# Kernel tuning notes

Hardware: AMD Instinct MI355X
Metric: run time of the kernel (lower is better)

The kernel has to match this reference:

```python
import jax, jax.numpy as jnp
import numpy as np

D_MODEL = 96
N_HEAD = 3
HEAD_DIM = D_MODEL // N_HEAD  # 32
D_FF = 2048
WIDTH = 65
HALF_W = (WIDTH - 1) // 2  # 32
EPS = 1e-5


def layer_norm(x, g, b):
    mu = jnp.mean(x, axis=-1, keepdims=True)
    var = jnp.mean(jnp.square(x - mu), axis=-1, keepdims=True)
    return (x - mu) * jax.lax.rsqrt(var + EPS) * g + b


def setup_inputs() -> dict:
    key = jax.random.key(0)
    ks = jax.random.split(key, 8)
    B, T = 8, 2048
    s = 0.05
    return {
        "x": jax.random.normal(ks[0], (B, D_MODEL, T), dtype=jnp.float32),
        "w_qkv": jax.random.normal(ks[1], (3 * D_MODEL, D_MODEL), dtype=jnp.float32) * s,
        "b_qkv": jnp.zeros((3 * D_MODEL,), dtype=jnp.float32),
        "w_out": jax.random.normal(ks[2], (D_MODEL, D_MODEL), dtype=jnp.float32) * s,
        "b_out": jnp.zeros((D_MODEL,), dtype=jnp.float32),
        "ln1_g": jnp.ones((D_MODEL,), dtype=jnp.float32),
        "ln1_b": jnp.zeros((D_MODEL,), dtype=jnp.float32),
        "w_ff1": jax.random.normal(ks[3], (D_FF, D_MODEL), dtype=jnp.float32) * s,
        "b_ff1": jnp.zeros((D_FF,), dtype=jnp.float32),
        "w_ff2": jax.random.normal(ks[4], (D_MODEL, D_FF), dtype=jnp.float32) * s,
        "b_ff2": jnp.zeros((D_MODEL,), dtype=jnp.float32),
        "ln2_g": jnp.ones((D_MODEL,), dtype=jnp.float32),
        "ln2_b": jnp.zeros((D_MODEL,), dtype=jnp.float32),
        "lnf_g": jnp.ones((D_MODEL,), dtype=jnp.float32),
        "lnf_b": jnp.zeros((D_MODEL,), dtype=jnp.float32),
    }


def reference(x, w_qkv, b_qkv, w_out, b_out, ln1_g, ln1_b, w_ff1, b_ff1,
              w_ff2, b_ff2, ln2_g, ln2_b, lnf_g, lnf_b):
    # x: (B, C, T) -> (B, T, C)
    h = jnp.transpose(x, (0, 2, 1))
    B, T, C = h.shape

    # --- multi-head self-attention with banded mask ---
    qkv = h @ w_qkv.T + b_qkv                      # (B, T, 3C)
    q, k, v = jnp.split(qkv, 3, axis=-1)
    q = q.reshape(B, T, N_HEAD, HEAD_DIM)
    k = k.reshape(B, T, N_HEAD, HEAD_DIM)
    v = v.reshape(B, T, N_HEAD, HEAD_DIM)

    scale = 1.0 / jnp.sqrt(jnp.float32(HEAD_DIM))
    scores = jnp.einsum("bthd,bshd->bhts", q, k) * scale  # (B, H, T, T)

    idx = jnp.arange(T)
    band = jnp.abs(idx[:, None] - idx[None, :]) <= HALF_W  # |i-j| <= half width
    scores = jnp.where(band[None, None], scores, jnp.float32(-jnp.inf))

    attn = jax.nn.softmax(scores, axis=-1)
    ctx = jnp.einsum("bhts,bshd->bthd", attn, v).reshape(B, T, C)
    attn_out = ctx @ w_out.T + b_out

    # --- post-norm encoder layer (dropout inactive / eval mode) ---
    h = layer_norm(h + attn_out, ln1_g, ln1_b)
    ff = jax.nn.relu(h @ w_ff1.T + b_ff1) @ w_ff2.T + b_ff2
    h = layer_norm(h + ff, ln2_g, ln2_b)

    # extra layernorm applied when width is not None
    h = layer_norm(h, lnf_g, lnf_b)

    # (B, T, C) -> (B, C, T)
    return jnp.transpose(h, (0, 2, 1))
```

## Files before the change

### kernel.cpp

```cpp
#include <hip/hip_runtime.h>
#include <hip/hip_bf16.h>

#define B 8
#define T 2048
#define C 96
#define NH 3
#define HD 32
#define FFD 2048
#define HALF_W 32
#define BT (B*T)

typedef __hip_bfloat16 bf16;
typedef __attribute__((ext_vector_type(8))) short short8;
typedef __attribute__((ext_vector_type(4))) short short4v;
typedef __attribute__((ext_vector_type(16))) float floatx16;

__device__ __forceinline__ short f2bs(float v){
    __hip_bfloat16 h = __float2bfloat16(v);
    return *reinterpret_cast<short*>(&h);
}
__device__ __forceinline__ int imin(int a, int b){ return a < b ? a : b; }
__device__ __forceinline__ int imax(int a, int b){ return a > b ? a : b; }
__device__ __forceinline__ short8 ld_b64x2(const short* p){
    short4v a = *(const short4v*)p;
    short4v b = *(const short4v*)(p + 4);
    short8 v;
    v[0]=a[0]; v[1]=a[1]; v[2]=a[2]; v[3]=a[3];
    v[4]=b[0]; v[5]=b[1]; v[6]=b[2]; v[7]=b[3];
    return v;
}

__global__ void cvtw_kernel(const float* __restrict__ wq, const float* __restrict__ wo,
                            const float* __restrict__ w1, const float* __restrict__ w2,
                            bf16* __restrict__ dst){
    int i = blockIdx.x*256 + threadIdx.x;
    if(i < 27648){
        int e = i&7, lane = (i>>3)&63, r = i>>9;
        int ks = r%6, ot = r/6;
        int o = ot*32 + (lane&31);
        int k = ks*16 + (lane>>5)*8 + e;
        dst[i] = __float2bfloat16(wq[o*96 + k]);
    } else if(i < 36864){
        int j = i - 27648;
        int e = j&7, lane = (j>>3)&63, r = j>>9;
        int ks = r%6, ct = r/6;
        int c = ct*32 + (lane&31);
        int k = ks*16 + (lane>>5)*8 + e;
        dst[i] = __float2bfloat16(wo[c*96 + k]);
    } else if(i < 233472){
        int j = i - 36864;
        int e = j&7, lane = (j>>3)&63, r = j>>9;
        int ks = r%6; r /= 6;
        int w = r%4, jt = r/4;
        int row = jt*128 + w*32 + (lane&31);
        int k = ks*16 + (lane>>5)*8 + e;
        dst[i] = __float2bfloat16(w1[row*96 + k]);
    } else if(i < 430080){
        int j = i - 233472;
        int e = j&7, lane = (j>>3)&63, r = j>>9;
        int ct = r%3; r /= 3;
        int g = r%2; r /= 2;
        int w = r%4, jt = r/4;
        int c = ct*32 + (lane&31);
        int k = jt*128 + w*32 + g*16 + (lane>>5)*8 + e;
        dst[i] = __float2bfloat16(w2[c*FFD + k]);
    }
}

__global__ __launch_bounds__(256) void qkv_kernel(
    const float* __restrict__ x, const bf16* __restrict__ wqs,
    const float* __restrict__ bias, bf16* __restrict__ qkvs){
    __shared__ float xs[96*36];
    int b  = blockIdx.x >> 6;
    int t0 = (blockIdx.x & 63) * 32;
    for(int e = threadIdx.x; e < 96*8; e += 256){
        int c = e >> 3, t4 = e & 7;
        *(float4*)(xs + c*36 + t4*4) =
            *(const float4*)(x + (size_t)b*C*T + (size_t)c*T + t0 + t4*4);
    }
    __syncthreads();
    int r0 = b*T + t0;
    const int w = threadIdx.x >> 6, lane = threadIdx.x & 63;
    const int lm = lane & 31, hq = lane >> 5;
    short8 bfr[6];
    #pragma unroll
    for(int ks = 0; ks < 6; ++ks){
        short8 v;
        #pragma unroll
        for(int i = 0; i < 8; ++i)
            v[i] = f2bs(xs[(ks*16 + hq*8 + i)*36 + lm]);
        bfr[ks] = v;
    }
    int nacc = (w == 0) ? 3 : 2;
    int ots[3] = {w, w+4, 8};
    floatx16 acc[3];
    #pragma unroll
    for(int i = 0; i < 3; ++i)
        #pragma unroll
        for(int r = 0; r < 16; ++r) acc[i][r] = 0.f;
    #pragma unroll
    for(int i = 0; i < 3; ++i){
        if(i < nacc){
            #pragma unroll
            for(int ks = 0; ks < 6; ++ks){
                short8 af = *(const short8*)((const short*)wqs
                              + (size_t)(ots[i]*6 + ks)*512 + lane*8);
                acc[i] = __builtin_amdgcn_mfma_f32_32x32x16_bf16(af, bfr[ks], acc[i], 0,0,0);
            }
        }
    }
    #pragma unroll
    for(int i = 0; i < 3; ++i){
        if(i < nacc){
            int type = ots[i]/3, hh = ots[i]%3;
            size_t rowbase = (((size_t)type*B*NH) + (size_t)b*NH + hh)*T + t0 + lm;
            #pragma unroll
            for(int q = 0; q < 4; ++q){
                float4 bv = *(const float4*)(bias + ots[i]*32 + 8*q + 4*hq);
                short4v pk;
                pk[0] = f2bs(acc[i][4*q+0] + bv.x);
                pk[1] = f2bs(acc[i][4*q+1] + bv.y);
                pk[2] = f2bs(acc[i][4*q+2] + bv.z);
                pk[3] = f2bs(acc[i][4*q+3] + bv.w);
                *(short4v*)((short*)qkvs + rowbase*32 + 8*q + 4*hq) = pk;
            }
        }
    }
}

__global__ __launch_bounds__(128) void attn_kernel(const bf16* __restrict__ qkvs,
                                                   bf16* __restrict__ ctxh){
    __shared__ __align__(16) short VtS[32*132];
    __shared__ __align__(16) short PtS[2][32*100];
    __shared__ float LsS[2][32];
    int blk = blockIdx.x;
    int ntile = T/64;
    int b   = blk / (NH*ntile);
    int rem = blk % (NH*ntile);
    int h   = rem / ntile;
    int t0  = (rem % ntile) * 64;
    const short* qb = (const short*)qkvs + ((size_t)0*B*NH + (size_t)b*NH + h)*T*32;
    const short* kb = (const short*)qkvs + ((size_t)1*B*NH + (size_t)b*NH + h)*T*32;
    const short* vb = (const short*)qkvs + ((size_t)2*B*NH + (size_t)b*NH + h)*T*32;
    const int tid = threadIdx.x;
    const int w = tid >> 6, lane = tid & 63;
    const int lm = lane & 31, hq = lane >> 5;

    for(int e = tid; e < 256; e += 128){
        int kp = e >> 2, d8 = e & 3;
        int sa = imin(imax(t0 - 32 + 2*kp, 0), T-1);
        int sb = imin(imax(t0 - 32 + 2*kp + 1, 0), T-1);
        short8 va = *(const short8*)(vb + (size_t)sa*32 + d8*8);
        short8 v2 = *(const short8*)(vb + (size_t)sb*32 + d8*8);
        #pragma unroll
        for(int j = 0; j < 8; ++j){
            int val = (int)(unsigned short)va[j] | ((int)(unsigned short)v2[j] << 16);
            *(int*)(VtS + (d8*8 + j)*132 + 2*kp) = val;
        }
    }
    short8 qf0, qf1;
    {
        const short* qrow = qb + (size_t)(t0 + 32*w + lm)*32;
        qf0 = *(const short8*)(qrow + hq*8);
        qf1 = *(const short8*)(qrow + 16 + hq*8);
    }
    floatx16 S[3];
    #pragma unroll
    for(int sub = 0; sub < 3; ++sub){
        int srow = imin(imax(t0 + 32*w - 32 + sub*32 + lm, 0), T-1);
        const short* krow = kb + (size_t)srow*32;
        short8 kf0 = *(const short8*)(krow + hq*8);
        short8 kf1 = *(const short8*)(krow + 16 + hq*8);
        floatx16 z;
        #pragma unroll
        for(int r = 0; r < 16; ++r) z[r] = 0.f;
        z = __builtin_amdgcn_mfma_f32_32x32x16_bf16(kf0, qf0, z, 0,0,0);
        z = __builtin_amdgcn_mfma_f32_32x32x16_bf16(kf1, qf1, z, 0,0,0);
        S[sub] = z;
    }
    const float scale = 0.17677669529663687f;
    float part = 0.f;
    #pragma unroll
    for(int sub = 0; sub < 3; ++sub){
        #pragma unroll
        for(int r = 0; r < 16; ++r){
            int key_local = sub*32 + (r&3) + 8*(r>>2) + 4*hq;
            int s_glob = t0 + 32*w - 32 + key_local;
            int rel = key_local - lm;
            bool ok = (rel >= 0) && (rel <= 64) && (s_glob >= 0) && (s_glob < T);
            float p = ok ? __expf(S[sub][r]*scale) : 0.f;
            S[sub][r] = p;
            part += p;
        }
    }
    float ltot = part + __shfl_xor(part, 32);
    if(hq == 0) LsS[w][lm] = ltot;
    #pragma unroll
    for(int sub = 0; sub < 3; ++sub){
        #pragma unroll
        for(int q4 = 0; q4 < 4; ++q4){
            int kbase = sub*32 + 8*q4 + 4*hq;
            short4v pk;
            pk[0] = f2bs(S[sub][4*q4+0]);
            pk[1] = f2bs(S[sub][4*q4+1]);
            pk[2] = f2bs(S[sub][4*q4+2]);
            pk[3] = f2bs(S[sub][4*q4+3]);
            *(short4v*)(PtS[w] + lm*100 + kbase) = pk;
        }
    }
    __syncthreads();
    floatx16 O;
    #pragma unroll
    for(int r = 0; r < 16; ++r) O[r] = 0.f;
    #pragma unroll
    for(int ks = 0; ks < 6; ++ks){
        short8 pa = ld_b64x2(PtS[w] + lm*100 + ks*16 + hq*8);
        short8 vf = ld_b64x2(VtS + lm*132 + 32*w + ks*16 + hq*8);
        O = __builtin_amdgcn_mfma_f32_32x32x16_bf16(pa, vf, O, 0,0,0);
    }
    #pragma unroll
    for(int r = 0; r < 16; ++r){
        int qr = (r&3) + 8*(r>>2) + 4*hq;
        float linv = 1.f / LsS[w][qr];
        ((short*)ctxh)[(((size_t)b*NH + h)*T + t0 + 32*w + qr)*32 + lm] = f2bs(O[r]*linv);
    }
}

__global__ __launch_bounds__(192) void outproj_ln_kernel(
    const bf16* __restrict__ ctxh, const bf16* __restrict__ wos,
    const float* __restrict__ bias, const float* __restrict__ x,
    const float* __restrict__ g1, const float* __restrict__ bb1,
    float* __restrict__ h1, bf16* __restrict__ h1b){
    __shared__ float red[2][3][32];
    const int ct = threadIdx.x >> 6, lane = threadIdx.x & 63;
    const int lm = lane & 31, hq = lane >> 5;
    const int r0 = blockIdx.x * 32;
    const int b = r0 / T, tloc = r0 % T;
    short8 bfr[6];
    #pragma unroll
    for(int ks = 0; ks < 6; ++ks){
        int off = ks*16 + hq*8;
        int hh = off >> 5, dd = off & 31;
        bfr[ks] = *(const short8*)((const short*)ctxh
                    + (((size_t)b*NH + hh)*T + tloc + lm)*32 + dd);
    }
    floatx16 acc;
    #pragma unroll
    for(int r = 0; r < 16; ++r) acc[r] = 0.f;
    #pragma unroll
    for(int ks = 0; ks < 6; ++ks){
        short8 af = *(const short8*)((const short*)wos
                      + (size_t)(ct*6 + ks)*512 + lane*8);
        acc = __builtin_amdgcn_mfma_f32_32x32x16_bf16(af, bfr[ks], acc, 0,0,0);
    }
    float vals[16];
    float p1 = 0.f, p2 = 0.f;
    #pragma unroll
    for(int q = 0; q < 4; ++q){
        int c = ct*32 + 8*q + 4*hq;
        float4 bv = *(const float4*)(bias + c);
        float bva[4] = {bv.x, bv.y, bv.z, bv.w};
        #pragma unroll
        for(int r = 0; r < 4; ++r){
            float xv = x[(size_t)b*C*T + (size_t)(c + r)*T + tloc + lm];
            float v = acc[4*q+r] + bva[r] + xv;
            vals[4*q+r] = v;
            p1 += v; p2 += v*v;
        }
    }
    p1 += __shfl_xor(p1, 32);
    p2 += __shfl_xor(p2, 32);
    if(hq == 0){ red[0][ct][lm] = p1; red[1][ct][lm] = p2; }
    __syncthreads();
    float s  = red[0][0][lm] + red[0][1][lm] + red[0][2][lm];
    float s2 = red[1][0][lm] + red[1][1][lm] + red[1][2][lm];
    float mu = s * (1.0f/96.0f);
    float rstd = rsqrtf(s2*(1.0f/96.0f) - mu*mu + 1e-5f);
    int row = r0 + lm;
    #pragma unroll
    for(int q = 0; q < 4; ++q){
        int c = ct*32 + 8*q + 4*hq;
        float4 gv = *(const float4*)(g1 + c);
        float4 bv = *(const float4*)(bb1 + c);
        float ga[4] = {gv.x, gv.y, gv.z, gv.w};
        float ba[4] = {bv.x, bv.y, bv.z, bv.w};
        float4 yo;
        float ya[4];
        #pragma unroll
        for(int r = 0; r < 4; ++r)
            ya[r] = (vals[4*q+r] - mu)*rstd*ga[r] + ba[r];
        yo.x = ya[0]; yo.y = ya[1]; yo.z = ya[2]; yo.w = ya[3];
        *(float4*)(h1 + (size_t)row*96 + c) = yo;
        short4v pk;
        #pragma unroll
        for(int r = 0; r < 4; ++r) pk[r] = f2bs(ya[r]);
        *(short4v*)((short*)h1b + (size_t)row*96 + c) = pk;
    }
}

__global__ __launch_bounds__(256, 2) void ff_ln_kernel(
    const bf16* __restrict__ h1b, const float* __restrict__ h1,
    const bf16* __restrict__ w1s, const float* __restrict__ b1,
    const bf16* __restrict__ w2s, const float* __restrict__ b2,
    const float* __restrict__ g2, const float* __restrict__ bt2,
    const float* __restrict__ gf, const float* __restrict__ btf,
    float* __restrict__ out){
    __shared__ float redp[9*1088];
    __shared__ float zt[96*33];
    const int tid = threadIdx.x;
    const int w = tid >> 6, lane = tid & 63;
    const int lm = lane & 31, hq = lane >> 5;
    const int r0 = blockIdx.x * 32;
    short8 hf[6];
    #pragma unroll
    for(int ks = 0; ks < 6; ++ks)
        hf[ks] = *(const short8*)((const short*)h1b
                   + (size_t)(r0 + lm)*96 + ks*16 + hq*8);
    floatx16 acc2[3];
    #pragma unroll
    for(int i = 0; i < 3; ++i)
        #pragma unroll
        for(int r = 0; r < 16; ++r) acc2[i][r] = 0.f;

    const short* w1p = (const short*)w1s + (size_t)w*6*512 + lane*8;
    const short* w2p = (const short*)w2s + (size_t)w*2*3*512 + lane*8;
    short8 cw1[6];
    #pragma unroll
    for(int ks = 0; ks < 6; ++ks)
        cw1[ks] = *(const short8*)(w1p + ks*512);

    #pragma unroll
    for(int jt = 0; jt < 16; ++jt){
        const int jn = (jt + 1) & 15;
        short8 nw1[6], w2f[6];
        #pragma unroll
        for(int ks = 0; ks < 6; ++ks)
            nw1[ks] = *(const short8*)(w1p + (size_t)jn*4*6*512 + ks*512);
        #pragma unroll
        for(int g = 0; g < 2; ++g)
            #pragma unroll
            for(int ct = 0; ct < 3; ++ct)
                w2f[g*3 + ct] = *(const short8*)(w2p
                                  + ((size_t)jt*4*2*3 + g*3 + ct)*512);
        floatx16 aA, aB;
        #pragma unroll
        for(int r = 0; r < 16; ++r){ aA[r] = 0.f; aB[r] = 0.f; }
        #pragma unroll
        for(int ks = 0; ks < 3; ++ks){
            aA = __builtin_amdgcn_mfma_f32_32x32x16_bf16(cw1[2*ks],   hf[2*ks],   aA, 0,0,0);
            aB = __builtin_amdgcn_mfma_f32_32x32x16_bf16(cw1[2*ks+1], hf[2*ks+1], aB, 0,0,0);
        }
        int pk[4][2];
        #pragma unroll
        for(int q = 0; q < 4; ++q){
            float4 bv = *(const float4*)(b1 + jt*128 + w*32 + 8*q + 4*hq);
            float bva[4] = {bv.x, bv.y, bv.z, bv.w};
            short4v t;
            #pragma unroll
            for(int r = 0; r < 4; ++r){
                float v = aA[4*q+r] + aB[4*q+r] + bva[r];
                t[r] = f2bs(v > 0.f ? v : 0.f);
            }
            int2 u = *(int2*)&t;
            pk[q][0] = u.x; pk[q][1] = u.y;
        }
        #pragma unroll
        for(int g = 0; g < 2; ++g){
            int a0 = pk[2*g][0],   a1 = pk[2*g][1];
            int b0 = pk[2*g+1][0], b1v = pk[2*g+1][1];
            int ra0 = __shfl_xor(a0, 32),  ra1 = __shfl_xor(a1, 32);
            int rb0 = __shfl_xor(b0, 32),  rb1 = __shfl_xor(b1v, 32);
            int4 sfi;
            sfi.x = hq ? rb0 : a0;
            sfi.y = hq ? rb1 : a1;
            sfi.z = hq ? b0  : ra0;
            sfi.w = hq ? b1v : ra1;
            short8 sf = *(short8*)&sfi;
            #pragma unroll
            for(int ct = 0; ct < 3; ++ct)
                acc2[ct] = __builtin_amdgcn_mfma_f32_32x32x16_bf16(w2f[g*3+ct], sf, acc2[ct], 0,0,0);
        }
        #pragma unroll
        for(int ks = 0; ks < 6; ++ks) cw1[ks] = nw1[ks];
    }
    __syncthreads();
    if(w > 0){
        #pragma unroll
        for(int ct = 0; ct < 3; ++ct)
            #pragma unroll
            for(int q = 0; q < 4; ++q)
                #pragma unroll
                for(int r = 0; r < 4; ++r)
                    redp[((w-1)*3 + ct)*1088 + lane*17 + 4*q + r] = acc2[ct][4*q+r];
    }
    __syncthreads();
    if(w == 0){
        float vals[48];
        float p1 = 0.f, p2 = 0.f;
        #pragma unroll
        for(int ct = 0; ct < 3; ++ct){
            #pragma unroll
            for(int q = 0; q < 4; ++q){
                int c = ct*32 + 8*q + 4*hq;
                float4 bv = *(const float4*)(b2 + c);
                float4 rs = *(const float4*)(h1 + (size_t)(r0 + lm)*96 + c);
                float bva[4] = {bv.x, bv.y, bv.z, bv.w};
                float rsa[4] = {rs.x, rs.y, rs.z, rs.w};
                #pragma unroll
                for(int r = 0; r < 4; ++r){
                    float v = acc2[ct][4*q+r]
                            + redp[(0*3 + ct)*1088 + lane*17 + 4*q + r]
                            + redp[(1*3 + ct)*1088 + lane*17 + 4*q + r]
                            + redp[(2*3 + ct)*1088 + lane*17 + 4*q + r]
                            + bva[r] + rsa[r];
                    vals[ct*16 + 4*q + r] = v;
                    p1 += v; p2 += v*v;
                }
            }
        }
        p1 += __shfl_xor(p1, 32);
        p2 += __shfl_xor(p2, 32);
        float mu = p1*(1.0f/96.0f);
        float rstd = rsqrtf(p2*(1.0f/96.0f) - mu*mu + 1e-5f);
        float q1 = 0.f, q2 = 0.f;
        #pragma unroll
        for(int ct = 0; ct < 3; ++ct){
            #pragma unroll
            for(int q = 0; q < 4; ++q){
                int c = ct*32 + 8*q + 4*hq;
                float4 gv = *(const float4*)(g2 + c);
                float4 bv = *(const float4*)(bt2 + c);
                float ga[4] = {gv.x, gv.y, gv.z, gv.w};
                float ba[4] = {bv.x, bv.y, bv.z, bv.w};
                #pragma unroll
                for(int r = 0; r < 4; ++r){
                    float y = (vals[ct*16+4*q+r] - mu)*rstd*ga[r] + ba[r];
                    vals[ct*16+4*q+r] = y;
                    q1 += y; q2 += y*y;
                }
            }
        }
        q1 += __shfl_xor(q1, 32);
        q2 += __shfl_xor(q2, 32);
        float mu2 = q1*(1.0f/96.0f);
        float rstd2 = rsqrtf(q2*(1.0f/96.0f) - mu2*mu2 + 1e-5f);
        #pragma unroll
        for(int ct = 0; ct < 3; ++ct){
            #pragma unroll
            for(int q = 0; q < 4; ++q){
                int c = ct*32 + 8*q + 4*hq;
                float4 gv = *(const float4*)(gf + c);
                float4 bv = *(const float4*)(btf + c);
                float ga[4] = {gv.x, gv.y, gv.z, gv.w};
                float ba[4] = {bv.x, bv.y, bv.z, bv.w};
                #pragma unroll
                for(int r = 0; r < 4; ++r)
                    zt[(c + r)*33 + lm] = (vals[ct*16+4*q+r] - mu2)*rstd2*ga[r] + ba[r];
            }
        }
    }
    __syncthreads();
    int bb  = r0 / T;
    int t0g = r0 % T;
    for(int e = tid; e < 96*32; e += 256){
        int c = e >> 5, tt = e & 31;
        out[(size_t)bb*C*T + (size_t)c*T + t0g + tt] = zt[c*33 + tt];
    }
}

extern "C" void kernel_launch(void* const* d_in, const int* in_sizes, int n_in,
                              void* d_out, int out_size, void* d_ws, size_t ws_size,
                              hipStream_t stream) {
    const float* x     = (const float*)d_in[0];
    const float* w_qkv = (const float*)d_in[1];
    const float* b_qkv = (const float*)d_in[2];
    const float* w_out = (const float*)d_in[3];
    const float* b_out = (const float*)d_in[4];
    const float* ln1_g = (const float*)d_in[5];
    const float* ln1_b = (const float*)d_in[6];
    const float* w_ff1 = (const float*)d_in[7];
    const float* b_ff1 = (const float*)d_in[8];
    const float* w_ff2 = (const float*)d_in[9];
    const float* b_ff2 = (const float*)d_in[10];
    const float* ln2_g = (const float*)d_in[11];
    const float* ln2_b = (const float*)d_in[12];
    const float* lnf_g = (const float*)d_in[13];
    const float* lnf_b = (const float*)d_in[14];
    float* out = (float*)d_out;

    char* wsb = (char*)d_ws;
    bf16*  qkvs  = (bf16*)wsb;
    bf16*  ctxh  = (bf16*)(wsb + 9437184);
    float* h1    = (float*)(wsb + 12582912);
    bf16*  h1b   = (bf16*)(wsb + 18874368);
    bf16*  wts   = (bf16*)(wsb + 22020096);
    bf16*  wqs   = wts;
    bf16*  wos   = wts + 27648;
    bf16*  w1s   = wts + 36864;
    bf16*  w2s   = wts + 233472;

    cvtw_kernel      <<<1680, 256, 0, stream>>>(w_qkv, w_out, w_ff1, w_ff2, wts);
    qkv_kernel       <<<BT/32, 256, 0, stream>>>(x, wqs, b_qkv, qkvs);
    attn_kernel      <<<B*NH*(T/64), 128, 0, stream>>>(qkvs, ctxh);
    outproj_ln_kernel<<<BT/32, 192, 0, stream>>>(ctxh, wos, b_out, x,
                                                 ln1_g, ln1_b, h1, h1b);
    ff_ln_kernel     <<<BT/32, 256, 0, stream>>>(h1b, h1, w1s, b_ff1, w2s, b_ff2,
                                                 ln2_g, ln2_b, lnf_g, lnf_b, out);
}
```

Before: 132.4 us.

## Fuse attention with output projection and LayerNorm, drop fp32 residual buffer

The attention kernel now handles all three heads for a 64-token tile in one 384-thread block. The context stays in shared memory and is fed straight into the output projection and first LayerNorm, which removes the separate outproj kernel and the global ctx round trip. The fp32 h1 buffer is dropped: the FF kernel now reads the residual from the bf16 h1b copy, which cuts memory traffic but lowers residual precision. The fused kernel has fewer blocks (256) with more shared memory each, which may reduce occupancy.

Result: faster. 128.8 us (-2.7%).

```diff
diff --git a/kernel.cpp b/kernel.cpp
--- a/kernel.cpp
+++ b/kernel.cpp
@@ -18,6 +18,10 @@
 __device__ __forceinline__ short f2bs(float v){
     __hip_bfloat16 h = __float2bfloat16(v);
     return *reinterpret_cast<short*>(&h);
+}
+__device__ __forceinline__ float bs2f(short s){
+    unsigned u = ((unsigned)(unsigned short)s) << 16;
+    return __uint_as_float(u);
 }
 __device__ __forceinline__ int imin(int a, int b){ return a < b ? a : b; }
 __device__ __forceinline__ int imax(int a, int b){ return a > b ? a : b; }
@@ -128,26 +132,27 @@
     }
 }
 
-__global__ __launch_bounds__(128) void attn_kernel(const bf16* __restrict__ qkvs,
-                                                   bf16* __restrict__ ctxh){
-    __shared__ __align__(16) short VtS[32*132];
-    __shared__ __align__(16) short PtS[2][32*100];
-    __shared__ float LsS[2][32];
-    int blk = blockIdx.x;
-    int ntile = T/64;
-    int b   = blk / (NH*ntile);
-    int rem = blk % (NH*ntile);
-    int h   = rem / ntile;
-    int t0  = (rem % ntile) * 64;
-    const short* qb = (const short*)qkvs + ((size_t)0*B*NH + (size_t)b*NH + h)*T*32;
-    const short* kb = (const short*)qkvs + ((size_t)1*B*NH + (size_t)b*NH + h)*T*32;
-    const short* vb = (const short*)qkvs + ((size_t)2*B*NH + (size_t)b*NH + h)*T*32;
+__global__ __launch_bounds__(384) void attn_op_kernel(
+    const bf16* __restrict__ qkvs, const bf16* __restrict__ wos,
+    const float* __restrict__ bias, const float* __restrict__ x,
+    const float* __restrict__ g1, const float* __restrict__ bb1,
+    bf16* __restrict__ h1b){
+    __shared__ __align__(16) short VtS[3*32*132];
+    __shared__ __align__(16) short PtS[6][3200];
+    __shared__ float LsS[6][32];
+    __shared__ __align__(16) short ctxS[64*100];
+    __shared__ float red1[2][6][32];
     const int tid = threadIdx.x;
-    const int w = tid >> 6, lane = tid & 63;
+    const int w = tid / 64, lane = tid & 63;
     const int lm = lane & 31, hq = lane >> 5;
-
-    for(int e = tid; e < 256; e += 128){
-        int kp = e >> 2, d8 = e & 3;
+    int b  = blockIdx.x >> 5;
+    int t0 = (blockIdx.x & 31) * 64;
+    const int h = w >> 1, half = w & 1;
+
+    for(int e = tid; e < 768; e += 384){
+        int hh = e / 256, rem = e & 255;
+        int kp = rem >> 2, d8 = rem & 3;
+        const short* vb = (const short*)qkvs + ((size_t)2*B*NH + (size_t)b*NH + hh)*T*32;
         int sa = imin(imax(t0 - 32 + 2*kp, 0), T-1);
         int sb = imin(imax(t0 - 32 + 2*kp + 1, 0), T-1);
         short8 va = *(const short8*)(vb + (size_t)sa*32 + d8*8);
@@ -155,19 +160,21 @@
         #pragma unroll
         for(int j = 0; j < 8; ++j){
             int val = (int)(unsigned short)va[j] | ((int)(unsigned short)v2[j] << 16);
-            *(int*)(VtS + (d8*8 + j)*132 + 2*kp) = val;
-        }
-    }
+            *(int*)(VtS + hh*32*132 + (d8*8 + j)*132 + 2*kp) = val;
+        }
+    }
+    const short* qb = (const short*)qkvs + ((size_t)0*B*NH + (size_t)b*NH + h)*T*32;
+    const short* kb = (const short*)qkvs + ((size_t)1*B*NH + (size_t)b*NH + h)*T*32;
     short8 qf0, qf1;
     {
-        const short* qrow = qb + (size_t)(t0 + 32*w + lm)*32;
+        const short* qrow = qb + (size_t)(t0 + 32*half + lm)*32;
         qf0 = *(const short8*)(qrow + hq*8);
         qf1 = *(const short8*)(qrow + 16 + hq*8);
     }
     floatx16 S[3];
     #pragma unroll
     for(int sub = 0; sub < 3; ++sub){
-        int srow = imin(imax(t0 + 32*w - 32 + sub*32 + lm, 0), T-1);
+        int srow = imin(imax(t0 + 32*half - 32 + sub*32 + lm, 0), T-1);
         const short* krow = kb + (size_t)srow*32;
         short8 kf0 = *(const short8*)(krow + hq*8);
         short8 kf1 = *(const short8*)(krow + 16 + hq*8);
@@ -185,7 +192,7 @@
         #pragma unroll
         for(int r = 0; r < 16; ++r){
             int key_local = sub*32 + (r&3) + 8*(r>>2) + 4*hq;
-            int s_glob = t0 + 32*w - 32 + key_local;
+            int s_glob = t0 + 32*half - 32 + key_local;
             int rel = key_local - lm;
             bool ok = (rel >= 0) && (rel <= 64) && (s_glob >= 0) && (s_glob < T);
             float p = ok ? __expf(S[sub][r]*scale) : 0.f;
@@ -215,35 +222,23 @@
     #pragma unroll
     for(int ks = 0; ks < 6; ++ks){
         short8 pa = ld_b64x2(PtS[w] + lm*100 + ks*16 + hq*8);
-        short8 vf = ld_b64x2(VtS + lm*132 + 32*w + ks*16 + hq*8);
+        short8 vf = ld_b64x2(VtS + h*32*132 + lm*132 + 32*half + ks*16 + hq*8);
         O = __builtin_amdgcn_mfma_f32_32x32x16_bf16(pa, vf, O, 0,0,0);
     }
     #pragma unroll
     for(int r = 0; r < 16; ++r){
         int qr = (r&3) + 8*(r>>2) + 4*hq;
         float linv = 1.f / LsS[w][qr];
-        ((short*)ctxh)[(((size_t)b*NH + h)*T + t0 + 32*w + qr)*32 + lm] = f2bs(O[r]*linv);
-    }
-}
-
-__global__ __launch_bounds__(192) void outproj_ln_kernel(
-    const bf16* __restrict__ ctxh, const bf16* __restrict__ wos,
-    const float* __restrict__ bias, const float* __restrict__ x,
-    const float* __restrict__ g1, const float* __restrict__ bb1,
-    float* __restrict__ h1, bf16* __restrict__ h1b){
-    __shared__ float red[2][3][32];
-    const int ct = threadIdx.x >> 6, lane = threadIdx.x & 63;
-    const int lm = lane & 31, hq = lane >> 5;
-    const int r0 = blockIdx.x * 32;
-    const int b = r0 / T, tloc = r0 % T;
+        ctxS[(32*half + qr)*100 + h*32 + lm] = f2bs(O[r]*linv);
+    }
+    __syncthreads();
+
+    const int mh = (w >= 3) ? 1 : 0;
+    const int ct = w - 3*mh;
     short8 bfr[6];
     #pragma unroll
-    for(int ks = 0; ks < 6; ++ks){
-        int off = ks*16 + hq*8;
-        int hh = off >> 5, dd = off & 31;
-        bfr[ks] = *(const short8*)((const short*)ctxh
-                    + (((size_t)b*NH + hh)*T + tloc + lm)*32 + dd);
-    }
+    for(int ks = 0; ks < 6; ++ks)
+        bfr[ks] = ld_b64x2(ctxS + (mh*32 + lm)*100 + ks*16 + hq*8);
     floatx16 acc;
     #pragma unroll
     for(int r = 0; r < 16; ++r) acc[r] = 0.f;
@@ -253,6 +248,7 @@
                       + (size_t)(ct*6 + ks)*512 + lane*8);
         acc = __builtin_amdgcn_mfma_f32_32x32x16_bf16(af, bfr[ks], acc, 0,0,0);
     }
+    const int tloc = t0 + mh*32;
     float vals[16];
     float p1 = 0.f, p2 = 0.f;
     #pragma unroll
@@ -270,13 +266,13 @@
     }
     p1 += __shfl_xor(p1, 32);
     p2 += __shfl_xor(p2, 32);
-    if(hq == 0){ red[0][ct][lm] = p1; red[1][ct][lm] = p2; }
-    __syncthreads();
-    float s  = red[0][0][lm] + red[0][1][lm] + red[0][2][lm];
-    float s2 = red[1][0][lm] + red[1][1][lm] + red[1][2][lm];
+    if(hq == 0){ red1[0][w][lm] = p1; red1[1][w][lm] = p2; }
+    __syncthreads();
+    float s  = red1[0][mh*3+0][lm] + red1[0][mh*3+1][lm] + red1[0][mh*3+2][lm];
+    float s2 = red1[1][mh*3+0][lm] + red1[1][mh*3+1][lm] + red1[1][mh*3+2][lm];
     float mu = s * (1.0f/96.0f);
     float rstd = rsqrtf(s2*(1.0f/96.0f) - mu*mu + 1e-5f);
-    int row = r0 + lm;
+    int row = b*T + tloc + lm;
     #pragma unroll
     for(int q = 0; q < 4; ++q){
         int c = ct*32 + 8*q + 4*hq;
@@ -284,22 +280,16 @@
         float4 bv = *(const float4*)(bb1 + c);
         float ga[4] = {gv.x, gv.y, gv.z, gv.w};
         float ba[4] = {bv.x, bv.y, bv.z, bv.w};
-        float4 yo;
-        float ya[4];
+        short4v pk;
         #pragma unroll
         for(int r = 0; r < 4; ++r)
-            ya[r] = (vals[4*q+r] - mu)*rstd*ga[r] + ba[r];
-        yo.x = ya[0]; yo.y = ya[1]; yo.z = ya[2]; yo.w = ya[3];
-        *(float4*)(h1 + (size_t)row*96 + c) = yo;
-        short4v pk;
-        #pragma unroll
-        for(int r = 0; r < 4; ++r) pk[r] = f2bs(ya[r]);
+            pk[r] = f2bs((vals[4*q+r] - mu)*rstd*ga[r] + ba[r]);
         *(short4v*)((short*)h1b + (size_t)row*96 + c) = pk;
     }
 }
 
 __global__ __launch_bounds__(256, 2) void ff_ln_kernel(
-    const bf16* __restrict__ h1b, const float* __restrict__ h1,
+    const bf16* __restrict__ h1b,
     const bf16* __restrict__ w1s, const float* __restrict__ b1,
     const bf16* __restrict__ w2s, const float* __restrict__ b2,
     const float* __restrict__ g2, const float* __restrict__ bt2,
@@ -403,16 +393,15 @@
             for(int q = 0; q < 4; ++q){
                 int c = ct*32 + 8*q + 4*hq;
                 float4 bv = *(const float4*)(b2 + c);
-                float4 rs = *(const float4*)(h1 + (size_t)(r0 + lm)*96 + c);
+                short4v hv = *(const short4v*)((const short*)h1b + (size_t)(r0 + lm)*96 + c);
                 float bva[4] = {bv.x, bv.y, bv.z, bv.w};
-                float rsa[4] = {rs.x, rs.y, rs.z, rs.w};
                 #pragma unroll
                 for(int r = 0; r < 4; ++r){
                     float v = acc2[ct][4*q+r]
                             + redp[(0*3 + ct)*1088 + lane*17 + 4*q + r]
                             + redp[(1*3 + ct)*1088 + lane*17 + 4*q + r]
                             + redp[(2*3 + ct)*1088 + lane*17 + 4*q + r]
-                            + bva[r] + rsa[r];
+                            + bva[r] + bs2f(hv[r]);
                     vals[ct*16 + 4*q + r] = v;
                     p1 += v; p2 += v*v;
                 }
@@ -490,20 +479,17 @@
 
     char* wsb = (char*)d_ws;
     bf16*  qkvs  = (bf16*)wsb;
-    bf16*  ctxh  = (bf16*)(wsb + 9437184);
-    float* h1    = (float*)(wsb + 12582912);
-    bf16*  h1b   = (bf16*)(wsb + 18874368);
-    bf16*  wts   = (bf16*)(wsb + 22020096);
+    bf16*  h1b   = (bf16*)(wsb + 9437184);
+    bf16*  wts   = (bf16*)(wsb + 12582912);
     bf16*  wqs   = wts;
     bf16*  wos   = wts + 27648;
     bf16*  w1s   = wts + 36864;
     bf16*  w2s   = wts + 233472;
 
-    cvtw_kernel      <<<1680, 256, 0, stream>>>(w_qkv, w_out, w_ff1, w_ff2, wts);
-    qkv_kernel       <<<BT/32, 256, 0, stream>>>(x, wqs, b_qkv, qkvs);
-    attn_kernel      <<<B*NH*(T/64), 128, 0, stream>>>(qkvs, ctxh);
-    outproj_ln_kernel<<<BT/32, 192, 0, stream>>>(ctxh, wos, b_out, x,
-                                                 ln1_g, ln1_b, h1, h1b);
-    ff_ln_kernel     <<<BT/32, 256, 0, stream>>>(h1b, h1, w1s, b_ff1, w2s, b_ff2,
-                                                 ln2_g, ln2_b, lnf_g, lnf_b, out);
-}
+    cvtw_kernel   <<<1680, 256, 0, stream>>>(w_qkv, w_out, w_ff1, w_ff2, wts);
+    qkv_kernel    <<<BT/32, 256, 0, stream>>>(x, wqs, b_qkv, qkvs);
+    attn_op_kernel<<<B*(T/64), 384, 0, stream>>>(qkvs, wos, b_out, x,
+                                                 ln1_g, ln1_b, h1b);
+    ff_ln_kernel  <<<BT/32, 256, 0, stream>>>(h1b, w1s, b_ff1, w2s, b_ff2,
+                                              ln2_g, ln2_b, lnf_g, lnf_b, out);
+}
```
